# Kernel optimization log

Measured on AMD Instinct MI355X. Metric: run time of the kernel, lower is better.

The kernel has to match this reference:

```python
import jax, jax.numpy as jnp
import numpy as np
import math

B, S, DM, H, DH = 2, 2048, 1024, 16, 64  # batch, seq, d_model, heads, head_dim


def setup_inputs() -> dict:
    key = jax.random.key(0)
    ks = jax.random.split(key, 4)
    scale = 0.02
    return {
        "hidden_states": jax.random.normal(ks[0], (B, S, DM), jnp.float32),
        "Wq": jax.random.normal(ks[1], (DM, DM), jnp.float32) * scale,
        "bq": jnp.zeros((DM,), jnp.float32),
        "Wk": jax.random.normal(ks[2], (DM, DM), jnp.float32) * scale,
        "bk": jnp.zeros((DM,), jnp.float32),
        "Wv": jax.random.normal(ks[3], (DM, DM), jnp.float32) * scale,
        "bv": jnp.zeros((DM,), jnp.float32),
    }


def reference(hidden_states, Wq, bq, Wk, bk, Wv, bv):
    b, s, _ = hidden_states.shape

    def proj(W, bias):
        # torch Linear: x @ W.T + b, then transpose_for_scores -> [B,H,S,Dh]
        x = hidden_states @ W.T + bias
        return x.reshape(b, s, H, DH).transpose(0, 2, 1, 3)

    query = proj(Wq, bq)
    key = proj(Wk, bk)
    value = proj(Wv, bv)

    # qk_matmul input calibration stats (abs-max over whole tensor)
    q_max = jax.lax.stop_gradient(jnp.max(jnp.abs(query)))
    kT_max = jax.lax.stop_gradient(jnp.max(jnp.abs(key)))  # transpose doesn't change abs-max

    attn_weights = jnp.einsum('bhqd,bhkd->bhqk', query, key)  # [B,H,S,S]
    qk_out_max = jax.lax.stop_gradient(jnp.max(jnp.abs(attn_weights)))

    attn_weights = attn_weights / math.sqrt(DH)
    attn_weights = jax.nn.softmax(attn_weights.astype(jnp.float32), axis=-1).astype(query.dtype)
    # eval mode: dropout p=0.0; head_mask is None

    # v_matmul input stats; note source also records attn_weights abs-max as 'v_matmul_out' (faithful)
    aw_max = jax.lax.stop_gradient(jnp.max(jnp.abs(attn_weights)))
    v_max = jax.lax.stop_gradient(jnp.max(jnp.abs(value)))
    v_out_max = aw_max  # source bug: re-reads attn_weights for v_matmul_out

    attn_output = jnp.einsum('bhqk,bhkd->bhqd', attn_weights, value)
    attn_output = attn_output.transpose(0, 2, 1, 3).reshape(b, s, H * DH)
    return attn_output, q_max, kT_max, qk_out_max, aw_max, v_max, v_out_max
```

## Files before the change

### kernel.cpp

```cpp
#include <hip/hip_runtime.h>
#include <hip/hip_bf16.h>
#include <stdint.h>

typedef __attribute__((ext_vector_type(8))) short short8;
typedef __attribute__((ext_vector_type(4))) short short4v;
typedef __attribute__((ext_vector_type(4))) float f32x4;

#define MFMA(a, b, c) __builtin_amdgcn_mfma_f32_16x16x32_bf16((a), (b), (c), 0, 0, 0)

#define C1 0.18033688011112042f
#define INV_C1 5.545177444479562f

static __device__ __forceinline__ unsigned int f2bf2(float x, float y) {
  union { __hip_bfloat162 h; unsigned int u; } c;
  c.h = __float22bfloat162_rn(make_float2(x, y));
  return c.u;
}

static __device__ __forceinline__ float exp2_fast(float x) {
  float r;
  asm("v_exp_f32 %0, %1" : "=v"(r) : "v"(x));
  return r;
}
static __device__ __forceinline__ unsigned int cvtpk(float lo, float hi) {
  unsigned int r;
  asm("v_cvt_pk_bf16_f32 %0, %1, %2" : "=v"(r) : "v"(lo), "v"(hi));
  return r;
}

static __device__ __forceinline__ void atomic_max_f32(float* addr, float v) {
  atomicMax((int*)addr, __float_as_int(v));
}

static __device__ __forceinline__ void gl_lds16(const void* g, void* l) {
  __builtin_amdgcn_global_load_lds(
      (const __attribute__((address_space(1))) void*)g,
      (__attribute__((address_space(3))) void*)l, 16, 0, 0);
}

__global__ __launch_bounds__(256) void k_cvt(
    const float* __restrict__ X, const float* __restrict__ Wq,
    const float* __restrict__ Wk, const float* __restrict__ Wv,
    short* __restrict__ Xb, short* __restrict__ Wb) {
  const int y = blockIdx.y;
  const int i = (blockIdx.x * 256 + threadIdx.x) * 8;
  const float* src;
  short* dstbase;
  if (y == 0) {
    if (i >= 4096 * 1024) return;
    src = X;
    dstbase = Xb;
  } else {
    if (i >= 1048576) return;
    src = (y == 1) ? Wq : (y == 2) ? Wk : Wv;
    dstbase = Wb + (y - 1) * 1048576;
  }
  const float4 a = *(const float4*)(src + i);
  const float4 b = *(const float4*)(src + i + 4);
  union { unsigned int u[4]; short8 s; } P;
  P.u[0] = f2bf2(a.x, a.y);
  P.u[1] = f2bf2(a.z, a.w);
  P.u[2] = f2bf2(b.x, b.y);
  P.u[3] = f2bf2(b.z, b.w);
  const int s = i >> 10, c0 = i & 1023;
  const int off = (((s >> 7) * 32 + (c0 >> 5)) * 4 + ((c0 >> 3) & 3)) * 1024 +
                  (s & 127) * 8;
  *(short8*)(dstbase + off) = P.s;
}

__global__ __launch_bounds__(256) void k_qkv(
    const short* __restrict__ Xb, const short* __restrict__ Wball,
    const float* __restrict__ bq, const float* __restrict__ bk,
    const float* __restrict__ bv,
    short* __restrict__ Qo, short* __restrict__ Ko, short* __restrict__ Vo,
    float* __restrict__ stats) {
  const int fid = (blockIdx.z * 32 + blockIdx.y) * 8 + blockIdx.x;
  const int sid = (fid & 7) * 96 + (fid >> 3);
  const int colb = sid & 7;
  const int zy = sid >> 3;
  const int z = zy >> 5;
  const int yb = zy & 31;

  const float* bias = (z == 0) ? bq : (z == 1) ? bk : bv;
  short* out = (z == 0) ? Qo : (z == 1) ? Ko : Vo;
  const bool qk = (z < 2);

  __shared__ __align__(16) short B0s[8192];
  __shared__ __align__(16) short B1s[8192];
  __shared__ __align__(16) short B2s[8192];
  __shared__ float red[4];

  const int t = threadIdx.x;
  const int lane = t & 63;
  const int w = t >> 6;
  const int l16 = lane & 15, quad = lane >> 4;
  const int wr = (w >> 1) * 64, wc = (w & 1) * 64;
  const int row0 = yb * 128;
  const int col0 = colb * 128;

  const short* ag = Xb + yb * 131072 + w * 512 + lane * 8;
  const short* bg = Wball + z * 1048576 + colb * 131072 + w * 512 + lane * 8;

  const int f0b = qk ? 4096 : 0, f0r = qk ? wc : wr;
  const int f1b = qk ? 0 : 4096, f1r = qk ? wr : wc;
  const int cq = quad * 1024;

  f32x4 acc[4][4];
#pragma unroll
  for (int i = 0; i < 4; ++i)
#pragma unroll
    for (int j = 0; j < 4; ++j) acc[i][j] = {0.f, 0.f, 0.f, 0.f};

#define STAGE(buf, ko_)                                  \
  do {                                                   \
    gl_lds16(ag + (ko_), (buf) + w * 512);               \
    gl_lds16(ag + (ko_) + 2048, (buf) + 2048 + w * 512); \
    gl_lds16(bg + (ko_), (buf) + 4096 + w * 512);        \
    gl_lds16(bg + (ko_) + 2048, (buf) + 6144 + w * 512); \
  } while (0)

#define COMPUTE(buf)                                                   \
  do {                                                                 \
    short8 fr0[4], fr1[4];                                             \
    _Pragma("unroll") for (int a = 0; a < 4; ++a)                      \
        fr0[a] = *(const short8*)&(buf)[f0b + cq + (f0r + a * 16 + l16) * 8]; \
    _Pragma("unroll") for (int b = 0; b < 4; ++b)                      \
        fr1[b] = *(const short8*)&(buf)[f1b + cq + (f1r + b * 16 + l16) * 8]; \
    _Pragma("unroll") for (int a = 0; a < 4; ++a)                      \
        _Pragma("unroll") for (int b = 0; b < 4; ++b)                  \
            acc[a][b] = MFMA(fr0[a], fr1[b], acc[a][b]);               \
  } while (0)

#define WAITBAR(n)                                                          \
  do {                                                                      \
    asm volatile("s_waitcnt lgkmcnt(0) vmcnt(" #n ")\n\ts_barrier" ::: "memory"); \
    __builtin_amdgcn_sched_barrier(0);                                      \
  } while (0)

  STAGE(B0s, 0);
  STAGE(B1s, 4096);
  WAITBAR(4);
  int ks = 8192;
#pragma unroll
  for (int i = 0; i < 10; ++i) {
    STAGE(B2s, ks); ks += 4096; COMPUTE(B0s); WAITBAR(4);
    STAGE(B0s, ks); ks += 4096; COMPUTE(B1s); WAITBAR(4);
    STAGE(B1s, ks); ks += 4096; COMPUTE(B2s); WAITBAR(4);
  }
  COMPUTE(B0s);
  WAITBAR(0);
  COMPUTE(B1s);
#undef STAGE
#undef COMPUTE
#undef WAITBAR

  const float qs = (z == 0) ? C1 : 1.0f;
  float amax = 0.f;
  if (qk) {
#pragma unroll
    for (int a = 0; a < 4; ++a) {
      const int dg = col0 + wc + a * 16 + quad * 4;
      const float4 b4 = *(const float4*)&bias[dg];
      const int h = dg >> 6, dl = dg & 63;
#pragma unroll
      for (int b = 0; b < 4; ++b) {
        const int sg = row0 + wr + b * 16 + l16;
        const float y0 = acc[a][b][0] + b4.x;
        const float y1 = acc[a][b][1] + b4.y;
        const float y2 = acc[a][b][2] + b4.z;
        const float y3 = acc[a][b][3] + b4.w;
        amax = fmaxf(amax, fmaxf(fmaxf(fabsf(y0), fabsf(y1)), fmaxf(fabsf(y2), fabsf(y3))));
        union { unsigned int u[2]; short4v s; } pk;
        pk.u[0] = cvtpk(y0 * qs, y1 * qs);
        pk.u[1] = cvtpk(y2 * qs, y3 * qs);
        const int bidx = sg >> 11, sl = sg & 2047;
        *(short4v*)&out[(size_t)(((bidx << 4) | h) * 2048 + sl) * 64 + dl] = pk.s;
      }
    }
  } else {
#pragma unroll
    for (int a = 0; a < 4; ++a) {
      const int sg = row0 + wr + a * 16 + quad * 4;
      const int bidx = sg >> 11, sl = sg & 2047;
#pragma unroll
      for (int b = 0; b < 4; ++b) {
        const int dg = col0 + wc + b * 16 + l16;
        const float bvf = bias[dg];
        const int h = dg >> 6, dl = dg & 63;
        const float y0 = acc[a][b][0] + bvf;
        const float y1 = acc[a][b][1] + bvf;
        const float y2 = acc[a][b][2] + bvf;
        const float y3 = acc[a][b][3] + bvf;
        amax = fmaxf(amax, fmaxf(fmaxf(fabsf(y0), fabsf(y1)), fmaxf(fabsf(y2), fabsf(y3))));
        union { unsigned int u[2]; short4v s; } pk;
        pk.u[0] = cvtpk(y0, y1);
        pk.u[1] = cvtpk(y2, y3);
        *(short4v*)&out[(size_t)(((bidx << 4) | h) * 64 + dl) * 2048 + sl] = pk.s;
      }
    }
  }
#pragma unroll
  for (int off = 32; off > 0; off >>= 1)
    amax = fmaxf(amax, __shfl_xor(amax, off, 64));
  if (lane == 0) red[w] = amax;
  __syncthreads();
  if (t == 0) {
    float m = fmaxf(fmaxf(red[0], red[1]), fmaxf(red[2], red[3]));
    atomic_max_f32(&stats[z], m);
  }
}

__global__ __launch_bounds__(512) void k_attn(
    const short* __restrict__ Q, const short* __restrict__ K,
    const short* __restrict__ V, float* __restrict__ O,
    float* __restrict__ stats) {
  const int fid = blockIdx.y * 16 + blockIdx.x;
  const int sid = ((fid & 7) << 6) + (fid >> 3);
  const int bh = sid >> 4;
  const int q0 = (sid & 15) << 7;
  const short* Qh = Q + (size_t)bh * 2048 * 64;
  const short* Kh = K + (size_t)bh * 2048 * 64;
  const short* Vh = V + (size_t)bh * 2048 * 64;

  __shared__ __align__(16) short Ks[2 * 4096];
  __shared__ __align__(16) short Vts[2 * 4096];
  __shared__ __align__(16) short Ps[8][16 * 64];
  __shared__ float redA[8], redB[8];

  const int t = threadIdx.x, lane = t & 63, w = t >> 6;
  const int l16 = lane & 15, quad = lane >> 4;
  const int srow = t >> 3;
  const int sslot = t & 7;
  const int wslot = (sslot ^ (srow & 7)) * 8;
  const int rsw = (l16 & 7);
  short* myPs = &Ps[w][0];

  short8 bq0, bq1;
  {
    const short* qsrc = Qh + (q0 + w * 16 + l16) * 64 + quad * 8;
    bq0 = *(const short8*)qsrc;
    bq1 = *(const short8*)(qsrc + 32);
  }

  float m_lane = -1e30f, l_lane = 0.f, xmin_lane = 1e30f;
  f32x4 o_acc[4];
#pragma unroll
  for (int jn = 0; jn < 4; ++jn) o_acc[jn] = {0.f, 0.f, 0.f, 0.f};
  const f32x4 zero = {0.f, 0.f, 0.f, 0.f};

  const int ksl0 = (quad ^ rsw) * 8;
  const int ksl1 = ((quad ^ rsw) ^ 4) * 8;

  short8 pk0 = *(const short8*)(Kh + srow * 64 + sslot * 8);
  short8 pv0 = *(const short8*)(Vh + srow * 2048 + sslot * 8);

  for (int kt = 0; kt < 32; ++kt) {
    const int bo = (kt & 1) << 12;
    asm volatile("s_waitcnt vmcnt(0)" ::: "memory");
    *(short8*)&Ks[bo + srow * 64 + wslot] = pk0;
    *(short8*)&Vts[bo + srow * 64 + wslot] = pv0;
    {
      const int ktn = (kt < 31) ? kt + 1 : 31;
      pk0 = *(const short8*)(Kh + (ktn * 64 + srow) * 64 + sslot * 8);
      pv0 = *(const short8*)(Vh + srow * 2048 + ktn * 64 + sslot * 8);
    }
    asm volatile("s_waitcnt lgkmcnt(0)\n\ts_barrier" ::: "memory");
    __builtin_amdgcn_sched_barrier(0);

    f32x4 sacc[4];
    __builtin_amdgcn_s_setprio(1);
#pragma unroll
    for (int j = 0; j < 4; ++j) {
      const int kb = bo + (j * 16 + l16) * 64;
      short8 kf0 = *(const short8*)&Ks[kb + ksl0];
      short8 kf1 = *(const short8*)&Ks[kb + ksl1];
      sacc[j] = MFMA(kf1, bq1, MFMA(kf0, bq0, zero));
    }
    __builtin_amdgcn_s_setprio(0);

    {
      float pmax = m_lane, psum = l_lane, xmn = xmin_lane;
#pragma unroll
      for (int j = 0; j < 4; ++j) {
        const float x0 = sacc[j][0], x1 = sacc[j][1];
        const float x2 = sacc[j][2], x3 = sacc[j][3];
        pmax = fmaxf(fmaxf(x0, fmaxf(x1, x2)), fmaxf(x3, pmax));
        xmn = fminf(fminf(x0, fminf(x1, x2)), fminf(x3, xmn));
        const float e0 = exp2_fast(x0), e1 = exp2_fast(x1);
        const float e2 = exp2_fast(x2), e3 = exp2_fast(x3);
        psum += (e0 + e1) + (e2 + e3);
        union { unsigned int u[2]; short4v s; } pk;
        pk.u[0] = cvtpk(e0, e1);
        pk.u[1] = cvtpk(e2, e3);
        *(short4v*)&myPs[l16 * 64 + ((j * 16 + quad * 4) ^ (rsw << 3))] = pk.s;
      }
      m_lane = pmax;
      l_lane = psum;
      xmin_lane = xmn;
    }
    asm volatile("" ::: "memory");

    __builtin_amdgcn_s_setprio(1);
#pragma unroll
    for (int tstep = 0; tstep < 2; ++tstep) {
      const int psl = (tstep * 32 + quad * 8) ^ (rsw << 3);
      short8 ap = *(const short8*)&myPs[l16 * 64 + psl];
#pragma unroll
      for (int jn = 0; jn < 4; ++jn) {
        short8 vf = *(const short8*)&Vts[bo + (jn * 16 + l16) * 64 + psl];
        o_acc[jn] = MFMA(ap, vf, o_acc[jn]);
      }
    }
    __builtin_amdgcn_s_setprio(0);
    asm volatile("" ::: "memory");
  }

  float l = l_lane;
  l += __shfl_xor(l, 16, 64);
  l += __shfl_xor(l, 32, 64);
  float m = m_lane;
  m = fmaxf(m, __shfl_xor(m, 16, 64));
  m = fmaxf(m, __shfl_xor(m, 32, 64));
  float xm = xmin_lane;
  xm = fminf(xm, __shfl_xor(xm, 16, 64));
  xm = fminf(xm, __shfl_xor(xm, 32, 64));
  float aw = exp2_fast(m) / l;
  float qkx = fmaxf(m, -xm);

  const int bidx = bh >> 4, h = bh & 15;
  float linv[4];
#pragma unroll
  for (int r = 0; r < 4; ++r)
    linv[r] = 1.0f / __shfl(l, quad * 4 + r, 16);
#pragma unroll
  for (int jn = 0; jn < 4; ++jn) {
    const int d = jn * 16 + l16;
#pragma unroll
    for (int r = 0; r < 4; ++r) {
      const int s_row = q0 + w * 16 + quad * 4 + r;
      O[((size_t)(bidx * 2048 + s_row) * 1024) + h * 64 + d] =
          o_acc[jn][r] * linv[r];
    }
  }

#pragma unroll
  for (int off = 32; off > 0; off >>= 1) {
    qkx = fmaxf(qkx, __shfl_xor(qkx, off, 64));
    aw = fmaxf(aw, __shfl_xor(aw, off, 64));
  }
  if (lane == 0) {
    redA[w] = qkx;
    redB[w] = aw;
  }
  __syncthreads();
  if (t == 0) {
    float a = redA[0], b = redB[0];
#pragma unroll
    for (int i = 1; i < 8; ++i) {
      a = fmaxf(a, redA[i]);
      b = fmaxf(b, redB[i]);
    }
    atomic_max_f32(&stats[3], a * INV_C1);
    atomic_max_f32(&stats[4], b);
  }
}

__global__ void k_fin(const float* __restrict__ stats, float* __restrict__ out) {
  const int i = threadIdx.x;
  if (i == 0) out[0] = stats[0];
  if (i == 1) out[1] = stats[1];
  if (i == 2) out[2] = stats[3];
  if (i == 3) out[3] = stats[4];
  if (i == 4) out[4] = stats[2];
  if (i == 5) out[5] = stats[4];
}

extern "C" void kernel_launch(void* const* d_in, const int* in_sizes, int n_in,
                              void* d_out, int out_size, void* d_ws, size_t ws_size,
                              hipStream_t stream) {
  const float* X = (const float*)d_in[0];
  const float* Wq = (const float*)d_in[1];
  const float* bq = (const float*)d_in[2];
  const float* Wk = (const float*)d_in[3];
  const float* bk = (const float*)d_in[4];
  const float* Wv = (const float*)d_in[5];
  const float* bv = (const float*)d_in[6];
  float* out = (float*)d_out;

  float* stats = (float*)d_ws;
  short* base = (short*)((char*)d_ws + 4096);
  short* Qb = base;
  short* Kb = base + 4194304;
  short* Vb = base + 8388608;
  short* Xb = base + 12582912;
  short* Wb = base + 16777216;

  k_cvt<<<dim3(2048, 4), 256, 0, stream>>>(X, Wq, Wk, Wv, Xb, Wb);
  k_qkv<<<dim3(8, 32, 3), 256, 0, stream>>>(Xb, Wb, bq, bk, bv, Qb, Kb, Vb, stats);
  k_attn<<<dim3(16, 32), 512, 0, stream>>>(Qb, Kb, Vb, out, stats);
  k_fin<<<1, 64, 0, stream>>>(stats, out + 4194304);
}
```

Measured before the change: 184.0 us.

## Process two query row groups per wave with 256-thread attention blocks

The attention kernel now runs 4 waves instead of 8 per block, and each wave handles 32 query rows as two 16-row groups. Each K fragment read from shared memory feeds two MFMAs, and each V fragment feeds two, halving LDS fragment reads per unit of work. Each thread also stages twice as many K/V vectors. The trade-off is higher register use per wave (two accumulator sets, two softmax states) and fewer waves available to hide latency.

```diff
diff --git a/kernel.cpp b/kernel.cpp
--- a/kernel.cpp
+++ b/kernel.cpp
@@ -210,7 +210,7 @@
   }
 }
 
-__global__ __launch_bounds__(512) void k_attn(
+__global__ __launch_bounds__(256) void k_attn(
     const short* __restrict__ Q, const short* __restrict__ K,
     const short* __restrict__ V, float* __restrict__ O,
     float* __restrict__ stats) {
@@ -224,66 +224,82 @@
 
   __shared__ __align__(16) short Ks[2 * 4096];
   __shared__ __align__(16) short Vts[2 * 4096];
-  __shared__ __align__(16) short Ps[8][16 * 64];
-  __shared__ float redA[8], redB[8];
+  __shared__ __align__(16) short Ps[4][32 * 64];
+  __shared__ float redA[4], redB[4];
 
   const int t = threadIdx.x, lane = t & 63, w = t >> 6;
   const int l16 = lane & 15, quad = lane >> 4;
-  const int srow = t >> 3;
-  const int sslot = t & 7;
-  const int wslot = (sslot ^ (srow & 7)) * 8;
+  const int srow = t >> 2;
+  const int scol = (t & 3) * 16;
+  const int sA = (t & 3) * 2;
+  const int wslotA = ((sA ^ (srow & 7)) * 8);
+  const int wslotB = (((sA + 1) ^ (srow & 7)) * 8);
   const int rsw = (l16 & 7);
   short* myPs = &Ps[w][0];
 
-  short8 bq0, bq1;
-  {
-    const short* qsrc = Qh + (q0 + w * 16 + l16) * 64 + quad * 8;
-    bq0 = *(const short8*)qsrc;
-    bq1 = *(const short8*)(qsrc + 32);
-  }
-
-  float m_lane = -1e30f, l_lane = 0.f, xmin_lane = 1e30f;
-  f32x4 o_acc[4];
-#pragma unroll
-  for (int jn = 0; jn < 4; ++jn) o_acc[jn] = {0.f, 0.f, 0.f, 0.f};
+  short8 bq8[2][2];
+#pragma unroll
+  for (int g = 0; g < 2; ++g) {
+    const short* qsrc = Qh + (q0 + w * 32 + g * 16 + l16) * 64 + quad * 8;
+    bq8[g][0] = *(const short8*)qsrc;
+    bq8[g][1] = *(const short8*)(qsrc + 32);
+  }
+
+  float m_lane[2] = {-1e30f, -1e30f}, l_lane[2] = {0.f, 0.f};
+  float xmin_lane[2] = {1e30f, 1e30f};
+  f32x4 o_acc[2][4];
+#pragma unroll
+  for (int g = 0; g < 2; ++g)
+#pragma unroll
+    for (int jn = 0; jn < 4; ++jn) o_acc[g][jn] = {0.f, 0.f, 0.f, 0.f};
   const f32x4 zero = {0.f, 0.f, 0.f, 0.f};
 
   const int ksl0 = (quad ^ rsw) * 8;
   const int ksl1 = ((quad ^ rsw) ^ 4) * 8;
 
-  short8 pk0 = *(const short8*)(Kh + srow * 64 + sslot * 8);
-  short8 pv0 = *(const short8*)(Vh + srow * 2048 + sslot * 8);
+  short8 pk0 = *(const short8*)(Kh + srow * 64 + scol);
+  short8 pk1 = *(const short8*)(Kh + srow * 64 + scol + 8);
+  short8 pv0 = *(const short8*)(Vh + srow * 2048 + scol);
+  short8 pv1 = *(const short8*)(Vh + srow * 2048 + scol + 8);
 
   for (int kt = 0; kt < 32; ++kt) {
     const int bo = (kt & 1) << 12;
     asm volatile("s_waitcnt vmcnt(0)" ::: "memory");
-    *(short8*)&Ks[bo + srow * 64 + wslot] = pk0;
-    *(short8*)&Vts[bo + srow * 64 + wslot] = pv0;
+    *(short8*)&Ks[bo + srow * 64 + wslotA] = pk0;
+    *(short8*)&Ks[bo + srow * 64 + wslotB] = pk1;
+    *(short8*)&Vts[bo + srow * 64 + wslotA] = pv0;
+    *(short8*)&Vts[bo + srow * 64 + wslotB] = pv1;
     {
       const int ktn = (kt < 31) ? kt + 1 : 31;
-      pk0 = *(const short8*)(Kh + (ktn * 64 + srow) * 64 + sslot * 8);
-      pv0 = *(const short8*)(Vh + srow * 2048 + ktn * 64 + sslot * 8);
+      const short* ksrc = Kh + (ktn * 64 + srow) * 64 + scol;
+      pk0 = *(const short8*)ksrc;
+      pk1 = *(const short8*)(ksrc + 8);
+      const short* vsrc = Vh + srow * 2048 + ktn * 64 + scol;
+      pv0 = *(const short8*)vsrc;
+      pv1 = *(const short8*)(vsrc + 8);
     }
     asm volatile("s_waitcnt lgkmcnt(0)\n\ts_barrier" ::: "memory");
     __builtin_amdgcn_sched_barrier(0);
 
-    f32x4 sacc[4];
+    f32x4 sacc[2][4];
     __builtin_amdgcn_s_setprio(1);
 #pragma unroll
     for (int j = 0; j < 4; ++j) {
       const int kb = bo + (j * 16 + l16) * 64;
       short8 kf0 = *(const short8*)&Ks[kb + ksl0];
       short8 kf1 = *(const short8*)&Ks[kb + ksl1];
-      sacc[j] = MFMA(kf1, bq1, MFMA(kf0, bq0, zero));
+      sacc[0][j] = MFMA(kf1, bq8[0][1], MFMA(kf0, bq8[0][0], zero));
+      sacc[1][j] = MFMA(kf1, bq8[1][1], MFMA(kf0, bq8[1][0], zero));
     }
     __builtin_amdgcn_s_setprio(0);
 
-    {
-      float pmax = m_lane, psum = l_lane, xmn = xmin_lane;
+#pragma unroll
+    for (int g = 0; g < 2; ++g) {
+      float pmax = m_lane[g], psum = l_lane[g], xmn = xmin_lane[g];
 #pragma unroll
       for (int j = 0; j < 4; ++j) {
-        const float x0 = sacc[j][0], x1 = sacc[j][1];
-        const float x2 = sacc[j][2], x3 = sacc[j][3];
+        const float x0 = sacc[g][j][0], x1 = sacc[g][j][1];
+        const float x2 = sacc[g][j][2], x3 = sacc[g][j][3];
         pmax = fmaxf(fmaxf(x0, fmaxf(x1, x2)), fmaxf(x3, pmax));
         xmn = fminf(fminf(x0, fminf(x1, x2)), fminf(x3, xmn));
         const float e0 = exp2_fast(x0), e1 = exp2_fast(x1);
@@ -292,11 +308,11 @@
         union { unsigned int u[2]; short4v s; } pk;
         pk.u[0] = cvtpk(e0, e1);
         pk.u[1] = cvtpk(e2, e3);
-        *(short4v*)&myPs[l16 * 64 + ((j * 16 + quad * 4) ^ (rsw << 3))] = pk.s;
+        *(short4v*)&myPs[(g * 16 + l16) * 64 + ((j * 16 + quad * 4) ^ (rsw << 3))] = pk.s;
       }
-      m_lane = pmax;
-      l_lane = psum;
-      xmin_lane = xmn;
+      m_lane[g] = pmax;
+      l_lane[g] = psum;
+      xmin_lane[g] = xmn;
     }
     asm volatile("" ::: "memory");
 
@@ -304,42 +320,56 @@
 #pragma unroll
     for (int tstep = 0; tstep < 2; ++tstep) {
       const int psl = (tstep * 32 + quad * 8) ^ (rsw << 3);
-      short8 ap = *(const short8*)&myPs[l16 * 64 + psl];
+      short8 ap0 = *(const short8*)&myPs[l16 * 64 + psl];
+      short8 ap1 = *(const short8*)&myPs[(16 + l16) * 64 + psl];
 #pragma unroll
       for (int jn = 0; jn < 4; ++jn) {
         short8 vf = *(const short8*)&Vts[bo + (jn * 16 + l16) * 64 + psl];
-        o_acc[jn] = MFMA(ap, vf, o_acc[jn]);
+        o_acc[0][jn] = MFMA(ap0, vf, o_acc[0][jn]);
+        o_acc[1][jn] = MFMA(ap1, vf, o_acc[1][jn]);
       }
     }
     __builtin_amdgcn_s_setprio(0);
     asm volatile("" ::: "memory");
   }
 
-  float l = l_lane;
-  l += __shfl_xor(l, 16, 64);
-  l += __shfl_xor(l, 32, 64);
-  float m = m_lane;
-  m = fmaxf(m, __shfl_xor(m, 16, 64));
-  m = fmaxf(m, __shfl_xor(m, 32, 64));
-  float xm = xmin_lane;
-  xm = fminf(xm, __shfl_xor(xm, 16, 64));
-  xm = fminf(xm, __shfl_xor(xm, 32, 64));
-  float aw = exp2_fast(m) / l;
-  float qkx = fmaxf(m, -xm);
+  float l_full[2], m_full[2], xm_full[2];
+#pragma unroll
+  for (int g = 0; g < 2; ++g) {
+    float l = l_lane[g];
+    l += __shfl_xor(l, 16, 64);
+    l += __shfl_xor(l, 32, 64);
+    l_full[g] = l;
+    float m = m_lane[g];
+    m = fmaxf(m, __shfl_xor(m, 16, 64));
+    m = fmaxf(m, __shfl_xor(m, 32, 64));
+    m_full[g] = m;
+    float xm = xmin_lane[g];
+    xm = fminf(xm, __shfl_xor(xm, 16, 64));
+    xm = fminf(xm, __shfl_xor(xm, 32, 64));
+    xm_full[g] = xm;
+  }
+  float aw = fmaxf(exp2_fast(m_full[0]) / l_full[0],
+                   exp2_fast(m_full[1]) / l_full[1]);
+  float qkx = fmaxf(fmaxf(m_full[0], -xm_full[0]),
+                    fmaxf(m_full[1], -xm_full[1]));
 
   const int bidx = bh >> 4, h = bh & 15;
-  float linv[4];
-#pragma unroll
-  for (int r = 0; r < 4; ++r)
-    linv[r] = 1.0f / __shfl(l, quad * 4 + r, 16);
-#pragma unroll
-  for (int jn = 0; jn < 4; ++jn) {
-    const int d = jn * 16 + l16;
-#pragma unroll
-    for (int r = 0; r < 4; ++r) {
-      const int s_row = q0 + w * 16 + quad * 4 + r;
-      O[((size_t)(bidx * 2048 + s_row) * 1024) + h * 64 + d] =
-          o_acc[jn][r] * linv[r];
+#pragma unroll
+  for (int g = 0; g < 2; ++g) {
+    float linv[4];
+#pragma unroll
+    for (int r = 0; r < 4; ++r)
+      linv[r] = 1.0f / __shfl(l_full[g], quad * 4 + r, 16);
+#pragma unroll
+    for (int jn = 0; jn < 4; ++jn) {
+      const int d = jn * 16 + l16;
+#pragma unroll
+      for (int r = 0; r < 4; ++r) {
+        const int s_row = q0 + w * 32 + g * 16 + quad * 4 + r;
+        O[((size_t)(bidx * 2048 + s_row) * 1024) + h * 64 + d] =
+            o_acc[g][jn][r] * linv[r];
+      }
     }
   }
 
@@ -354,12 +384,8 @@
   }
   __syncthreads();
   if (t == 0) {
-    float a = redA[0], b = redB[0];
-#pragma unroll
-    for (int i = 1; i < 8; ++i) {
-      a = fmaxf(a, redA[i]);
-      b = fmaxf(b, redB[i]);
-    }
+    float a = fmaxf(fmaxf(redA[0], redA[1]), fmaxf(redA[2], redA[3]));
+    float b = fmaxf(fmaxf(redB[0], redB[1]), fmaxf(redB[2], redB[3]));
     atomic_max_f32(&stats[3], a * INV_C1);
     atomic_max_f32(&stats[4], b);
   }
@@ -397,6 +423,6 @@
 
   k_cvt<<<dim3(2048, 4), 256, 0, stream>>>(X, Wq, Wk, Wv, Xb, Wb);
   k_qkv<<<dim3(8, 32, 3), 256, 0, stream>>>(Xb, Wb, bq, bk, bv, Qb, Kb, Vb, stats);
-  k_attn<<<dim3(16, 32), 512, 0, stream>>>(Qb, Kb, Vb, out, stats);
+  k_attn<<<dim3(16, 32), 256, 0, stream>>>(Qb, Kb, Vb, out, stats);
   k_fin<<<1, 64, 0, stream>>>(stats, out + 4194304);
 }
```

New measurement: 187.9 us. 1.02x slower.
